# Kernel optimization log

Measured on AMD Instinct MI355X. Metric: run time of the kernel, lower is better.

The kernel has to match this reference:

```python
import jax, jax.numpy as jnp
import numpy as np

B, D, H1, H2, E, O = 32768, 256, 512, 256, 16, 64


def setup_inputs() -> dict:
    key = jax.random.key(0)
    ks = jax.random.split(key, 12)
    s = lambda fan_in: 1.0 / np.sqrt(fan_in)
    return {
        "x": jax.random.normal(ks[0], (B, D), dtype=jnp.float32),
        "gate_w": jax.random.normal(ks[1], (D, E), dtype=jnp.float32) * s(D),
        "gate_b": jnp.zeros((E,), dtype=jnp.float32),
        "W1": jax.random.normal(ks[2], (E, D, H1), dtype=jnp.float32) * s(D),
        "b1": jnp.zeros((E, H1), dtype=jnp.float32),
        "W2": jax.random.normal(ks[3], (E, H1, H2), dtype=jnp.float32) * s(H1),
        "b2": jnp.zeros((E, H2), dtype=jnp.float32),
        "W3": jax.random.normal(ks[4], (E, H2, O), dtype=jnp.float32) * s(H2),
        "b3": jnp.zeros((E, O), dtype=jnp.float32),
        "head_w": jax.random.normal(ks[5], (O, 1), dtype=jnp.float32) * s(O),
        "head_b": jnp.zeros((1,), dtype=jnp.float32),
    }


def reference(x, gate_w, gate_b, W1, b1, W2, b2, W3, b3, head_w, head_b):
    # gating: softmax over experts, [B, E]
    gates = jax.nn.softmax(x @ gate_w + gate_b, axis=-1)
    # all-expert dense MLP as batched GEMMs over leading expert axis
    h1 = jax.nn.relu(jnp.einsum('bd,edh->ebh', x, W1) + b1[:, None, :])   # [E,B,H1]
    h2 = jax.nn.relu(jnp.einsum('ebh,ehk->ebk', h1, W2) + b2[:, None, :])  # [E,B,H2]
    eo = jnp.einsum('ebk,eko->ebo', h2, W3) + b3[:, None, :]               # [E,B,O]
    # gated combination: sum_e gates[b,e] * eo[e,b,:]
    fused = jnp.einsum('be,ebo->bo', gates, eo)                            # [B,O]
    yts = (fused @ head_w + head_b)[:, 0]                                  # [B]
    return yts
```

## Files before the change

kernel.cpp:

```cpp
#include <hip/hip_runtime.h>

#define B_TOK 32768
#define D_IN  256
#define H1D   512
#define H2D   256
#define NE    16
#define NO    64

typedef _Float16 half8 __attribute__((ext_vector_type(8)));
typedef _Float16 half4 __attribute__((ext_vector_type(4)));
typedef float   float4_t __attribute__((ext_vector_type(4)));

__global__ void pack_w1(const float* __restrict__ W1, _Float16* __restrict__ w1p) {
  int t = blockIdx.x * 256 + threadIdx.x;
  int lane = t & 63;
  int kt   = (t >> 6) & 7;
  int ntg  = (t >> 9) & 31;
  int e    = t >> 14;
  int n  = ntg * 16 + (lane & 15);
  int kb = kt * 32 + (lane >> 4) * 8;
  half8 v;
  #pragma unroll
  for (int j = 0; j < 8; ++j)
    v[j] = (_Float16)W1[((size_t)(e * D_IN + kb + j)) * H1D + n];
  *(half8*)(w1p + (size_t)t * 8) = v;
}

__global__ void pack_w2(const float* __restrict__ W2, _Float16* __restrict__ w2p) {
  int t = blockIdx.x * 256 + threadIdx.x;
  int lane = t & 63;
  int ktg  = (t >> 6) & 15;
  int ntg  = (t >> 10) & 15;
  int e    = t >> 14;
  int n  = ntg * 16 + (lane & 15);
  int kb = ktg * 32 + (lane >> 4) * 8;
  half8 v;
  #pragma unroll
  for (int j = 0; j < 8; ++j)
    v[j] = (_Float16)W2[((size_t)(e * H1D + kb + j)) * H2D + n];
  *(half8*)(w2p + (size_t)t * 8) = v;
}

__global__ void pack_gate(const float* __restrict__ gw, _Float16* __restrict__ gwp) {
  int t = threadIdx.x;
  int lane = t & 63;
  int kt   = t >> 6;
  int e  = lane & 15;
  int kb = kt * 32 + (lane >> 4) * 8;
  half8 v;
  #pragma unroll
  for (int j = 0; j < 8; ++j)
    v[j] = (_Float16)gw[(kb + j) * NE + e];
  *(half8*)(gwp + (size_t)t * 8) = v;
}

__global__ void w3h_kernel(const float* __restrict__ W3, const float* __restrict__ b3,
                           const float* __restrict__ hw, float* __restrict__ w3h,
                           float* __restrict__ c3) {
  int t = blockIdx.x * 256 + threadIdx.x;
  if (t < NE * H2D) {
    int e = t >> 8, h = t & 255;
    float s = 0.f;
    #pragma unroll
    for (int o = 0; o < NO; ++o) s = fmaf(W3[((size_t)(e * H2D + h)) * NO + o], hw[o], s);
    w3h[t] = s;
  } else if (t < NE * H2D + NE) {
    int e = t - NE * H2D;
    float s = 0.f;
    #pragma unroll
    for (int o = 0; o < NO; ++o) s = fmaf(b3[e * NO + o], hw[o], s);
    c3[e] = s;
  }
}

#define H1STR 520

__global__ __launch_bounds__(256, 2) void moe_main(
    const float* __restrict__ x,
    const float* __restrict__ b1,
    const float* __restrict__ b2,
    const _Float16* __restrict__ w1p,
    const _Float16* __restrict__ w2p,
    const _Float16* __restrict__ gwp,
    const float* __restrict__ gb,
    const float* __restrict__ w3h,
    const float* __restrict__ c3,
    const float* __restrict__ head_b,
    float* __restrict__ out) {
  __shared__ _Float16 h1_lds[64 * H1STR];
  __shared__ float g_lds[NE * 68];
  __shared__ float fin[4 * 64];

  const int tid  = threadIdx.x;
  const int w    = tid >> 6;
  const int lane = tid & 63;
  const int q    = lane >> 4;
  const int l16  = lane & 15;
  const int m0   = blockIdx.x * 64;
  const int tok_lane = (l16 >> 2) * 16 + q * 4 + (l16 & 3);

  half8 xf[4][8];
  #pragma unroll
  for (int nt = 0; nt < 4; ++nt) {
    const float* xr = x + (size_t)(m0 + nt * 16 + l16) * D_IN + q * 8;
    #pragma unroll
    for (int kt = 0; kt < 8; ++kt) {
      float4_t v0 = *(const float4_t*)(xr + kt * 32);
      float4_t v1 = *(const float4_t*)(xr + kt * 32 + 4);
      half8 h;
      h[0] = (_Float16)v0[0]; h[1] = (_Float16)v0[1];
      h[2] = (_Float16)v0[2]; h[3] = (_Float16)v0[3];
      h[4] = (_Float16)v1[0]; h[5] = (_Float16)v1[1];
      h[6] = (_Float16)v1[2]; h[7] = (_Float16)v1[3];
      xf[nt][kt] = h;
    }
  }

  {
    float gbv = gb[l16];
    #pragma unroll
    for (int mt = 0; mt < 4; ++mt) {
      if (mt == w) {
        float4_t lg = (float4_t){0.f, 0.f, 0.f, 0.f};
        #pragma unroll
        for (int kt = 0; kt < 8; ++kt) {
          half8 bfr = *(const half8*)(gwp + (size_t)kt * 512 + lane * 8);
          lg = __builtin_amdgcn_mfma_f32_16x16x32_f16(xf[mt][kt], bfr, lg, 0, 0, 0);
        }
        #pragma unroll
        for (int r = 0; r < 4; ++r) {
          float v = lg[r] + gbv;
          float m = v;
          m = fmaxf(m, __shfl_xor(m, 1));
          m = fmaxf(m, __shfl_xor(m, 2));
          m = fmaxf(m, __shfl_xor(m, 4));
          m = fmaxf(m, __shfl_xor(m, 8));
          float p = __expf(v - m);
          float s = p;
          s += __shfl_xor(s, 1);
          s += __shfl_xor(s, 2);
          s += __shfl_xor(s, 4);
          s += __shfl_xor(s, 8);
          g_lds[l16 * 68 + mt * 16 + q * 4 + r] = p / s;
        }
      }
    }
  }

  float yacc = 0.f;

  for (int e = 0; e < NE; ++e) {
    #pragma unroll
    for (int ch = 0; ch < 2; ++ch) {
      float4_t a1[4][4];
      #pragma unroll
      for (int mt = 0; mt < 4; ++mt)
        #pragma unroll
        for (int nt = 0; nt < 4; ++nt)
          a1[mt][nt] = (float4_t){0.f, 0.f, 0.f, 0.f};

      const _Float16* wbase =
          w1p + ((size_t)((e * 32 + ch * 16 + w * 4) * 8)) * 512 + lane * 8;
      #pragma unroll
      for (int kt = 0; kt < 8; ++kt) {
        half8 wc[4];
        #pragma unroll
        for (int mt = 0; mt < 4; ++mt)
          wc[mt] = *(const half8*)(wbase + (size_t)(mt * 8 + kt) * 512);
        #pragma unroll
        for (int mt = 0; mt < 4; ++mt)
          #pragma unroll
          for (int nt = 0; nt < 4; ++nt)
            a1[mt][nt] = __builtin_amdgcn_mfma_f32_16x16x32_f16(
                wc[mt], xf[nt][kt], a1[mt][nt], 0, 0, 0);
      }

      #pragma unroll
      for (int mt = 0; mt < 4; ++mt) {
        int colbase = ch * 256 + (w * 4 + mt) * 16 + q * 4;
        float4_t bb = *(const float4_t*)(b1 + e * H1D + colbase);
        #pragma unroll
        for (int nt = 0; nt < 4; ++nt) {
          half4 hv;
          #pragma unroll
          for (int r = 0; r < 4; ++r)
            hv[r] = (_Float16)fmaxf(a1[mt][nt][r] + bb[r], 0.f);
          *(half4*)(h1_lds + (nt * 16 + l16) * H1STR + colbase) = hv;
        }
      }
    }
    __syncthreads();

    float4_t h2[4][4];
    #pragma unroll
    for (int mt = 0; mt < 4; ++mt)
      #pragma unroll
      for (int nt = 0; nt < 4; ++nt)
        h2[mt][nt] = (float4_t){0.f, 0.f, 0.f, 0.f};

    const _Float16* w2base =
        w2p + ((size_t)((e * 16 + w * 4) * 16)) * 512 + lane * 8;
    #pragma unroll
    for (int kt = 0; kt < 16; ++kt) {
      half8 w2c[4];
      #pragma unroll
      for (int nt = 0; nt < 4; ++nt)
        w2c[nt] = *(const half8*)(w2base + (size_t)(nt * 16 + kt) * 512);
      half8 hac[4];
      #pragma unroll
      for (int mt = 0; mt < 4; ++mt)
        hac[mt] = *(const half8*)(h1_lds + (mt * 16 + l16) * H1STR + kt * 32 + q * 8);
      #pragma unroll
      for (int mt = 0; mt < 4; ++mt)
        #pragma unroll
        for (int nt = 0; nt < 4; ++nt)
          h2[mt][nt] = __builtin_amdgcn_mfma_f32_16x16x32_f16(
              hac[mt], w2c[nt], h2[mt][nt], 0, 0, 0);
    }

    float b2v[4], w3v[4];
    #pragma unroll
    for (int nt = 0; nt < 4; ++nt) {
      int n = w * 64 + nt * 16 + l16;
      b2v[nt] = b2[e * H2D + n];
      w3v[nt] = w3h[e * H2D + n];
    }
    float s[4][4];
    #pragma unroll
    for (int mt = 0; mt < 4; ++mt)
      #pragma unroll
      for (int r = 0; r < 4; ++r) s[mt][r] = 0.f;
    #pragma unroll
    for (int mt = 0; mt < 4; ++mt)
      #pragma unroll
      for (int nt = 0; nt < 4; ++nt)
        #pragma unroll
        for (int r = 0; r < 4; ++r)
          s[mt][r] += fmaxf(h2[mt][nt][r] + b2v[nt], 0.f) * w3v[nt];

    float ge = g_lds[e * 68 + tok_lane];
    #pragma unroll
    for (int i = 0; i < 16; ++i) {
      float v = s[i >> 2][i & 3];
      v += __shfl_xor(v, 1);
      v += __shfl_xor(v, 2);
      v += __shfl_xor(v, 4);
      v += __shfl_xor(v, 8);
      if (l16 == i) yacc += ge * v;
    }
    __syncthreads();
  }

  fin[w * 64 + tok_lane] = yacc;
  __syncthreads();
  if (tid < 64) {
    float sum = fin[tid] + fin[64 + tid] + fin[128 + tid] + fin[192 + tid];
    float gc = 0.f;
    #pragma unroll
    for (int e = 0; e < NE; ++e) gc += g_lds[e * 68 + tid] * c3[e];
    out[m0 + tid] = sum + gc + head_b[0];
  }
}

extern "C" void kernel_launch(void* const* d_in, const int* in_sizes, int n_in,
                              void* d_out, int out_size, void* d_ws, size_t ws_size,
                              hipStream_t stream) {
  const float* x      = (const float*)d_in[0];
  const float* gate_w = (const float*)d_in[1];
  const float* gate_b = (const float*)d_in[2];
  const float* W1     = (const float*)d_in[3];
  const float* b1     = (const float*)d_in[4];
  const float* W2     = (const float*)d_in[5];
  const float* b2     = (const float*)d_in[6];
  const float* W3     = (const float*)d_in[7];
  const float* b3     = (const float*)d_in[8];
  const float* head_w = (const float*)d_in[9];
  const float* head_b = (const float*)d_in[10];
  float* out = (float*)d_out;

  char* ws = (char*)d_ws;
  _Float16* w1p = (_Float16*)(ws);
  _Float16* w2p = (_Float16*)(ws + 4194304);
  _Float16* gwp = (_Float16*)(ws + 8388608);
  float*    w3h = (float*)(ws + 8396800);
  float*    c3  = (float*)(ws + 8413184);

  hipLaunchKernelGGL(pack_w1, dim3(1024), dim3(256), 0, stream, W1, w1p);
  hipLaunchKernelGGL(pack_w2, dim3(1024), dim3(256), 0, stream, W2, w2p);
  hipLaunchKernelGGL(pack_gate, dim3(1), dim3(512), 0, stream, gate_w, gwp);
  hipLaunchKernelGGL(w3h_kernel, dim3(17), dim3(256), 0, stream,
                     W3, b3, head_w, w3h, c3);
  hipLaunchKernelGGL(moe_main, dim3(B_TOK / 64), dim3(256), 0, stream,
                     x, b1, b2, w1p, w2p, gwp, gate_b, w3h, c3, head_b, out);
}
```

Baseline: 412.4 us.

## Use eight waves per block with double-buffered H1 and register prefetch

```diff
diff --git a/kernel.cpp b/kernel.cpp
--- a/kernel.cpp
+++ b/kernel.cpp
@@ -75,7 +75,7 @@
 
 #define H1STR 520
 
-__global__ __launch_bounds__(256, 2) void moe_main(
+__global__ __launch_bounds__(512, 2) void moe_main(
     const float* __restrict__ x,
     const float* __restrict__ b1,
     const float* __restrict__ b2,
@@ -87,9 +87,9 @@
     const float* __restrict__ c3,
     const float* __restrict__ head_b,
     float* __restrict__ out) {
-  __shared__ _Float16 h1_lds[64 * H1STR];
+  __shared__ _Float16 h1_lds[2][64 * H1STR];
   __shared__ float g_lds[NE * 68];
-  __shared__ float fin[4 * 64];
+  __shared__ float fin[8 * 64];
 
   const int tid  = threadIdx.x;
   const int w    = tid >> 6;
@@ -116,7 +116,7 @@
     }
   }
 
-  {
+  if (w < 4) {
     float gbv = gb[l16];
     #pragma unroll
     for (int mt = 0; mt < 4; ++mt) {
@@ -149,79 +149,99 @@
 
   float yacc = 0.f;
 
+  const _Float16* w1base = w1p + ((size_t)(w * 4 * 8)) * 512 + lane * 8;
+  const _Float16* w2base = w2p + ((size_t)(w * 2 * 16)) * 512 + lane * 8;
+
   for (int e = 0; e < NE; ++e) {
-    #pragma unroll
-    for (int ch = 0; ch < 2; ++ch) {
-      float4_t a1[4][4];
+    _Float16* h1b = h1_lds[e & 1];
+    const _Float16* w1e = w1base + (size_t)e * (32 * 8 * 512);
+    const _Float16* w2e = w2base + (size_t)e * (16 * 16 * 512);
+
+    float4_t a1[4][4];
+    #pragma unroll
+    for (int mt = 0; mt < 4; ++mt)
+      #pragma unroll
+      for (int nt = 0; nt < 4; ++nt)
+        a1[mt][nt] = (float4_t){0.f, 0.f, 0.f, 0.f};
+
+    half8 wc[4], wn[4];
+    #pragma unroll
+    for (int mt = 0; mt < 4; ++mt)
+      wc[mt] = *(const half8*)(w1e + (size_t)(mt * 8 + 0) * 512);
+    #pragma unroll
+    for (int kt = 0; kt < 8; ++kt) {
+      if (kt < 7) {
+        #pragma unroll
+        for (int mt = 0; mt < 4; ++mt)
+          wn[mt] = *(const half8*)(w1e + (size_t)(mt * 8 + kt + 1) * 512);
+      }
       #pragma unroll
       for (int mt = 0; mt < 4; ++mt)
         #pragma unroll
         for (int nt = 0; nt < 4; ++nt)
-          a1[mt][nt] = (float4_t){0.f, 0.f, 0.f, 0.f};
-
-      const _Float16* wbase =
-          w1p + ((size_t)((e * 32 + ch * 16 + w * 4) * 8)) * 512 + lane * 8;
-      #pragma unroll
-      for (int kt = 0; kt < 8; ++kt) {
-        half8 wc[4];
+          a1[mt][nt] = __builtin_amdgcn_mfma_f32_16x16x32_f16(
+              wc[mt], xf[nt][kt], a1[mt][nt], 0, 0, 0);
+      #pragma unroll
+      for (int mt = 0; mt < 4; ++mt) wc[mt] = wn[mt];
+    }
+
+    #pragma unroll
+    for (int mt = 0; mt < 4; ++mt) {
+      int colbase = (w * 4 + mt) * 16 + q * 4;
+      float4_t bb = *(const float4_t*)(b1 + e * H1D + colbase);
+      #pragma unroll
+      for (int nt = 0; nt < 4; ++nt) {
+        half4 hv;
+        #pragma unroll
+        for (int r = 0; r < 4; ++r)
+          hv[r] = (_Float16)fmaxf(a1[mt][nt][r] + bb[r], 0.f);
+        *(half4*)(h1b + (nt * 16 + l16) * H1STR + colbase) = hv;
+      }
+    }
+
+    __syncthreads();
+
+    float4_t h2[4][2];
+    #pragma unroll
+    for (int mt = 0; mt < 4; ++mt)
+      #pragma unroll
+      for (int nt = 0; nt < 2; ++nt)
+        h2[mt][nt] = (float4_t){0.f, 0.f, 0.f, 0.f};
+
+    half8 w2c[2], w2n[2], hac[4], han[4];
+    #pragma unroll
+    for (int nt = 0; nt < 2; ++nt)
+      w2c[nt] = *(const half8*)(w2e + (size_t)(nt * 16 + 0) * 512);
+    #pragma unroll
+    for (int mt = 0; mt < 4; ++mt)
+      hac[mt] = *(const half8*)(h1b + (mt * 16 + l16) * H1STR + 0 * 32 + q * 8);
+
+    #pragma unroll
+    for (int kt = 0; kt < 16; ++kt) {
+      if (kt < 15) {
+        #pragma unroll
+        for (int nt = 0; nt < 2; ++nt)
+          w2n[nt] = *(const half8*)(w2e + (size_t)(nt * 16 + kt + 1) * 512);
         #pragma unroll
         for (int mt = 0; mt < 4; ++mt)
-          wc[mt] = *(const half8*)(wbase + (size_t)(mt * 8 + kt) * 512);
-        #pragma unroll
-        for (int mt = 0; mt < 4; ++mt)
-          #pragma unroll
-          for (int nt = 0; nt < 4; ++nt)
-            a1[mt][nt] = __builtin_amdgcn_mfma_f32_16x16x32_f16(
-                wc[mt], xf[nt][kt], a1[mt][nt], 0, 0, 0);
+          han[mt] = *(const half8*)(h1b + (mt * 16 + l16) * H1STR + (kt + 1) * 32 + q * 8);
       }
-
-      #pragma unroll
-      for (int mt = 0; mt < 4; ++mt) {
-        int colbase = ch * 256 + (w * 4 + mt) * 16 + q * 4;
-        float4_t bb = *(const float4_t*)(b1 + e * H1D + colbase);
-        #pragma unroll
-        for (int nt = 0; nt < 4; ++nt) {
-          half4 hv;
-          #pragma unroll
-          for (int r = 0; r < 4; ++r)
-            hv[r] = (_Float16)fmaxf(a1[mt][nt][r] + bb[r], 0.f);
-          *(half4*)(h1_lds + (nt * 16 + l16) * H1STR + colbase) = hv;
-        }
-      }
-    }
-    __syncthreads();
-
-    float4_t h2[4][4];
-    #pragma unroll
-    for (int mt = 0; mt < 4; ++mt)
-      #pragma unroll
-      for (int nt = 0; nt < 4; ++nt)
-        h2[mt][nt] = (float4_t){0.f, 0.f, 0.f, 0.f};
-
-    const _Float16* w2base =
-        w2p + ((size_t)((e * 16 + w * 4) * 16)) * 512 + lane * 8;
-    #pragma unroll
-    for (int kt = 0; kt < 16; ++kt) {
-      half8 w2c[4];
-      #pragma unroll
-      for (int nt = 0; nt < 4; ++nt)
-        w2c[nt] = *(const half8*)(w2base + (size_t)(nt * 16 + kt) * 512);
-      half8 hac[4];
       #pragma unroll
       for (int mt = 0; mt < 4; ++mt)
-        hac[mt] = *(const half8*)(h1_lds + (mt * 16 + l16) * H1STR + kt * 32 + q * 8);
-      #pragma unroll
-      for (int mt = 0; mt < 4; ++mt)
-        #pragma unroll
-        for (int nt = 0; nt < 4; ++nt)
+        #pragma unroll
+        for (int nt = 0; nt < 2; ++nt)
           h2[mt][nt] = __builtin_amdgcn_mfma_f32_16x16x32_f16(
               hac[mt], w2c[nt], h2[mt][nt], 0, 0, 0);
-    }
-
-    float b2v[4], w3v[4];
-    #pragma unroll
-    for (int nt = 0; nt < 4; ++nt) {
-      int n = w * 64 + nt * 16 + l16;
+      #pragma unroll
+      for (int nt = 0; nt < 2; ++nt) w2c[nt] = w2n[nt];
+      #pragma unroll
+      for (int mt = 0; mt < 4; ++mt) hac[mt] = han[mt];
+    }
+
+    float b2v[2], w3v[2];
+    #pragma unroll
+    for (int nt = 0; nt < 2; ++nt) {
+      int n = w * 32 + nt * 16 + l16;
       b2v[nt] = b2[e * H2D + n];
       w3v[nt] = w3h[e * H2D + n];
     }
@@ -233,7 +253,7 @@
     #pragma unroll
     for (int mt = 0; mt < 4; ++mt)
       #pragma unroll
-      for (int nt = 0; nt < 4; ++nt)
+      for (int nt = 0; nt < 2; ++nt)
         #pragma unroll
         for (int r = 0; r < 4; ++r)
           s[mt][r] += fmaxf(h2[mt][nt][r] + b2v[nt], 0.f) * w3v[nt];
@@ -248,13 +268,14 @@
       v += __shfl_xor(v, 8);
       if (l16 == i) yacc += ge * v;
     }
-    __syncthreads();
   }
 
   fin[w * 64 + tok_lane] = yacc;
   __syncthreads();
   if (tid < 64) {
-    float sum = fin[tid] + fin[64 + tid] + fin[128 + tid] + fin[192 + tid];
+    float sum = 0.f;
+    #pragma unroll
+    for (int k = 0; k < 8; ++k) sum += fin[k * 64 + tid];
     float gc = 0.f;
     #pragma unroll
     for (int e = 0; e < NE; ++e) gc += g_lds[e * 68 + tid] * c3[e];
@@ -290,6 +311,6 @@
   hipLaunchKernelGGL(pack_gate, dim3(1), dim3(512), 0, stream, gate_w, gwp);
   hipLaunchKernelGGL(w3h_kernel, dim3(17), dim3(256), 0, stream,
                      W3, b3, head_w, w3h, c3);
-  hipLaunchKernelGGL(moe_main, dim3(B_TOK / 64), dim3(256), 0, stream,
+  hipLaunchKernelGGL(moe_main, dim3(B_TOK / 64), dim3(512), 0, stream,
                      x, b1, b2, w1p, w2p, gwp, gate_b, w3h, c3, head_b, out);
 }
```

Result: slower. 485.4 us (+17.7%).

## Use 128-token tiles with 16-wave blocks and merge prep kernels

Applied to the files above, without the earlier changes.

```diff
diff --git a/kernel.cpp b/kernel.cpp
--- a/kernel.cpp
+++ b/kernel.cpp
@@ -6,76 +6,79 @@
 #define H2D   256
 #define NE    16
 #define NO    64
+#define TK    128
 
 typedef _Float16 half8 __attribute__((ext_vector_type(8)));
 typedef _Float16 half4 __attribute__((ext_vector_type(4)));
 typedef float   float4_t __attribute__((ext_vector_type(4)));
 
-__global__ void pack_w1(const float* __restrict__ W1, _Float16* __restrict__ w1p) {
-  int t = blockIdx.x * 256 + threadIdx.x;
-  int lane = t & 63;
-  int kt   = (t >> 6) & 7;
-  int ntg  = (t >> 9) & 31;
-  int e    = t >> 14;
-  int n  = ntg * 16 + (lane & 15);
-  int kb = kt * 32 + (lane >> 4) * 8;
-  half8 v;
-  #pragma unroll
-  for (int j = 0; j < 8; ++j)
-    v[j] = (_Float16)W1[((size_t)(e * D_IN + kb + j)) * H1D + n];
-  *(half8*)(w1p + (size_t)t * 8) = v;
+__global__ void prep_kernel(const float* __restrict__ W1, const float* __restrict__ W2,
+                            const float* __restrict__ W3, const float* __restrict__ b3,
+                            const float* __restrict__ hw, const float* __restrict__ gw,
+                            _Float16* __restrict__ w1p, _Float16* __restrict__ w2p,
+                            float* __restrict__ w3h, float* __restrict__ c3,
+                            _Float16* __restrict__ gwp) {
+  int blk = blockIdx.x;
+  int tid = threadIdx.x;
+  if (blk < 1024) {
+    int t = blk * 256 + tid;
+    int lane = t & 63;
+    int kt   = (t >> 6) & 7;
+    int ntg  = (t >> 9) & 31;
+    int e    = t >> 14;
+    int n  = ntg * 16 + (lane & 15);
+    int kb = kt * 32 + (lane >> 4) * 8;
+    half8 v;
+    #pragma unroll
+    for (int j = 0; j < 8; ++j)
+      v[j] = (_Float16)W1[((size_t)(e * D_IN + kb + j)) * H1D + n];
+    *(half8*)(w1p + (size_t)t * 8) = v;
+  } else if (blk < 2048) {
+    int t = (blk - 1024) * 256 + tid;
+    int lane = t & 63;
+    int ktg  = (t >> 6) & 15;
+    int ntg  = (t >> 10) & 15;
+    int e    = t >> 14;
+    int n  = ntg * 16 + (lane & 15);
+    int kb = ktg * 32 + (lane >> 4) * 8;
+    half8 v;
+    #pragma unroll
+    for (int j = 0; j < 8; ++j)
+      v[j] = (_Float16)W2[((size_t)(e * H1D + kb + j)) * H2D + n];
+    *(half8*)(w2p + (size_t)t * 8) = v;
+  } else if (blk < 2065) {
+    int t = (blk - 2048) * 256 + tid;
+    if (t < NE * H2D) {
+      int e = t >> 8, h = t & 255;
+      float s = 0.f;
+      #pragma unroll
+      for (int o = 0; o < NO; ++o) s = fmaf(W3[((size_t)(e * H2D + h)) * NO + o], hw[o], s);
+      w3h[t] = s;
+    } else if (t < NE * H2D + NE) {
+      int e = t - NE * H2D;
+      float s = 0.f;
+      #pragma unroll
+      for (int o = 0; o < NO; ++o) s = fmaf(b3[e * NO + o], hw[o], s);
+      c3[e] = s;
+    }
+  } else {
+    for (int t = tid; t < 512; t += 256) {
+      int lane = t & 63;
+      int kt   = t >> 6;
+      int e  = lane & 15;
+      int kb = kt * 32 + (lane >> 4) * 8;
+      half8 v;
+      #pragma unroll
+      for (int j = 0; j < 8; ++j)
+        v[j] = (_Float16)gw[(kb + j) * NE + e];
+      *(half8*)(gwp + (size_t)t * 8) = v;
+    }
+  }
 }
 
-__global__ void pack_w2(const float* __restrict__ W2, _Float16* __restrict__ w2p) {
-  int t = blockIdx.x * 256 + threadIdx.x;
-  int lane = t & 63;
-  int ktg  = (t >> 6) & 15;
-  int ntg  = (t >> 10) & 15;
-  int e    = t >> 14;
-  int n  = ntg * 16 + (lane & 15);
-  int kb = ktg * 32 + (lane >> 4) * 8;
-  half8 v;
-  #pragma unroll
-  for (int j = 0; j < 8; ++j)
-    v[j] = (_Float16)W2[((size_t)(e * H1D + kb + j)) * H2D + n];
-  *(half8*)(w2p + (size_t)t * 8) = v;
-}
-
-__global__ void pack_gate(const float* __restrict__ gw, _Float16* __restrict__ gwp) {
-  int t = threadIdx.x;
-  int lane = t & 63;
-  int kt   = t >> 6;
-  int e  = lane & 15;
-  int kb = kt * 32 + (lane >> 4) * 8;
-  half8 v;
-  #pragma unroll
-  for (int j = 0; j < 8; ++j)
-    v[j] = (_Float16)gw[(kb + j) * NE + e];
-  *(half8*)(gwp + (size_t)t * 8) = v;
-}
-
-__global__ void w3h_kernel(const float* __restrict__ W3, const float* __restrict__ b3,
-                           const float* __restrict__ hw, float* __restrict__ w3h,
-                           float* __restrict__ c3) {
-  int t = blockIdx.x * 256 + threadIdx.x;
-  if (t < NE * H2D) {
-    int e = t >> 8, h = t & 255;
-    float s = 0.f;
-    #pragma unroll
-    for (int o = 0; o < NO; ++o) s = fmaf(W3[((size_t)(e * H2D + h)) * NO + o], hw[o], s);
-    w3h[t] = s;
-  } else if (t < NE * H2D + NE) {
-    int e = t - NE * H2D;
-    float s = 0.f;
-    #pragma unroll
-    for (int o = 0; o < NO; ++o) s = fmaf(b3[e * NO + o], hw[o], s);
-    c3[e] = s;
-  }
-}
-
 #define H1STR 520
 
-__global__ __launch_bounds__(256, 2) void moe_main(
+__global__ __launch_bounds__(1024, 4) void moe_main(
     const float* __restrict__ x,
     const float* __restrict__ b1,
     const float* __restrict__ b2,
@@ -87,22 +90,23 @@
     const float* __restrict__ c3,
     const float* __restrict__ head_b,
     float* __restrict__ out) {
-  __shared__ _Float16 h1_lds[64 * H1STR];
-  __shared__ float g_lds[NE * 68];
-  __shared__ float fin[4 * 64];
+  __shared__ _Float16 h1_lds[TK * H1STR];
+  __shared__ float g_lds[TK * 17];
+  __shared__ float fin[4 * TK];
 
   const int tid  = threadIdx.x;
   const int w    = tid >> 6;
   const int lane = tid & 63;
   const int q    = lane >> 4;
   const int l16  = lane & 15;
-  const int m0   = blockIdx.x * 64;
-  const int tok_lane = (l16 >> 2) * 16 + q * 4 + (l16 & 3);
-
-  half8 xf[4][8];
+  const int tp   = w >> 2;
+  const int ng   = w & 3;
+  const int m0   = blockIdx.x * TK;
+
+  half8 xf[2][8];
   #pragma unroll
-  for (int nt = 0; nt < 4; ++nt) {
-    const float* xr = x + (size_t)(m0 + nt * 16 + l16) * D_IN + q * 8;
+  for (int mi = 0; mi < 2; ++mi) {
+    const float* xr = x + (size_t)(m0 + (2 * tp + mi) * 16 + l16) * D_IN + q * 8;
     #pragma unroll
     for (int kt = 0; kt < 8; ++kt) {
       float4_t v0 = *(const float4_t*)(xr + kt * 32);
@@ -112,152 +116,157 @@
       h[2] = (_Float16)v0[2]; h[3] = (_Float16)v0[3];
       h[4] = (_Float16)v1[0]; h[5] = (_Float16)v1[1];
       h[6] = (_Float16)v1[2]; h[7] = (_Float16)v1[3];
-      xf[nt][kt] = h;
-    }
-  }
-
-  {
+      xf[mi][kt] = h;
+    }
+  }
+
+  if (ng == 0) {
     float gbv = gb[l16];
     #pragma unroll
-    for (int mt = 0; mt < 4; ++mt) {
-      if (mt == w) {
-        float4_t lg = (float4_t){0.f, 0.f, 0.f, 0.f};
-        #pragma unroll
-        for (int kt = 0; kt < 8; ++kt) {
-          half8 bfr = *(const half8*)(gwp + (size_t)kt * 512 + lane * 8);
-          lg = __builtin_amdgcn_mfma_f32_16x16x32_f16(xf[mt][kt], bfr, lg, 0, 0, 0);
-        }
-        #pragma unroll
-        for (int r = 0; r < 4; ++r) {
-          float v = lg[r] + gbv;
-          float m = v;
-          m = fmaxf(m, __shfl_xor(m, 1));
-          m = fmaxf(m, __shfl_xor(m, 2));
-          m = fmaxf(m, __shfl_xor(m, 4));
-          m = fmaxf(m, __shfl_xor(m, 8));
-          float p = __expf(v - m);
-          float s = p;
-          s += __shfl_xor(s, 1);
-          s += __shfl_xor(s, 2);
-          s += __shfl_xor(s, 4);
-          s += __shfl_xor(s, 8);
-          g_lds[l16 * 68 + mt * 16 + q * 4 + r] = p / s;
-        }
-      }
-    }
-  }
-
-  float yacc = 0.f;
+    for (int mi = 0; mi < 2; ++mi) {
+      float4_t lg = (float4_t){0.f, 0.f, 0.f, 0.f};
+      #pragma unroll
+      for (int kt = 0; kt < 8; ++kt) {
+        half8 bfr = *(const half8*)(gwp + (size_t)kt * 512 + lane * 8);
+        lg = __builtin_amdgcn_mfma_f32_16x16x32_f16(xf[mi][kt], bfr, lg, 0, 0, 0);
+      }
+      #pragma unroll
+      for (int r = 0; r < 4; ++r) {
+        float v = lg[r] + gbv;
+        float m = v;
+        m = fmaxf(m, __shfl_xor(m, 1));
+        m = fmaxf(m, __shfl_xor(m, 2));
+        m = fmaxf(m, __shfl_xor(m, 4));
+        m = fmaxf(m, __shfl_xor(m, 8));
+        float p = __expf(v - m);
+        float s = p;
+        s += __shfl_xor(s, 1);
+        s += __shfl_xor(s, 2);
+        s += __shfl_xor(s, 4);
+        s += __shfl_xor(s, 8);
+        int tok = (2 * tp + mi) * 16 + q * 4 + r;
+        g_lds[tok * 17 + l16] = p / s;
+      }
+    }
+  }
+
+  float yacc[2][4];
+  #pragma unroll
+  for (int mi = 0; mi < 2; ++mi)
+    #pragma unroll
+    for (int r = 0; r < 4; ++r) yacc[mi][r] = 0.f;
 
   for (int e = 0; e < NE; ++e) {
     #pragma unroll
-    for (int ch = 0; ch < 2; ++ch) {
-      float4_t a1[4][4];
-      #pragma unroll
-      for (int mt = 0; mt < 4; ++mt)
+    for (int nh = 0; nh < 2; ++nh) {
+      float4_t a1[2][4];
+      #pragma unroll
+      for (int mi = 0; mi < 2; ++mi)
         #pragma unroll
         for (int nt = 0; nt < 4; ++nt)
-          a1[mt][nt] = (float4_t){0.f, 0.f, 0.f, 0.f};
-
-      const _Float16* wbase =
-          w1p + ((size_t)((e * 32 + ch * 16 + w * 4) * 8)) * 512 + lane * 8;
+          a1[mi][nt] = (float4_t){0.f, 0.f, 0.f, 0.f};
+
+      const _Float16* w1e =
+          w1p + ((size_t)((e * 32 + ng * 8 + nh * 4) * 8)) * 512 + lane * 8;
       #pragma unroll
       for (int kt = 0; kt < 8; ++kt) {
         half8 wc[4];
         #pragma unroll
-        for (int mt = 0; mt < 4; ++mt)
-          wc[mt] = *(const half8*)(wbase + (size_t)(mt * 8 + kt) * 512);
-        #pragma unroll
-        for (int mt = 0; mt < 4; ++mt)
+        for (int nt = 0; nt < 4; ++nt)
+          wc[nt] = *(const half8*)(w1e + (size_t)(nt * 8 + kt) * 512);
+        #pragma unroll
+        for (int mi = 0; mi < 2; ++mi)
           #pragma unroll
           for (int nt = 0; nt < 4; ++nt)
-            a1[mt][nt] = __builtin_amdgcn_mfma_f32_16x16x32_f16(
-                wc[mt], xf[nt][kt], a1[mt][nt], 0, 0, 0);
-      }
-
-      #pragma unroll
-      for (int mt = 0; mt < 4; ++mt) {
-        int colbase = ch * 256 + (w * 4 + mt) * 16 + q * 4;
+            a1[mi][nt] = __builtin_amdgcn_mfma_f32_16x16x32_f16(
+                wc[nt], xf[mi][kt], a1[mi][nt], 0, 0, 0);
+      }
+
+      #pragma unroll
+      for (int nt = 0; nt < 4; ++nt) {
+        int colbase = (ng * 8 + nh * 4 + nt) * 16 + q * 4;
         float4_t bb = *(const float4_t*)(b1 + e * H1D + colbase);
         #pragma unroll
-        for (int nt = 0; nt < 4; ++nt) {
+        for (int mi = 0; mi < 2; ++mi) {
           half4 hv;
           #pragma unroll
           for (int r = 0; r < 4; ++r)
-            hv[r] = (_Float16)fmaxf(a1[mt][nt][r] + bb[r], 0.f);
-          *(half4*)(h1_lds + (nt * 16 + l16) * H1STR + colbase) = hv;
+            hv[r] = (_Float16)fmaxf(a1[mi][nt][r] + bb[r], 0.f);
+          *(half4*)(h1_lds + ((2 * tp + mi) * 16 + l16) * H1STR + colbase) = hv;
         }
       }
     }
+
     __syncthreads();
 
-    float4_t h2[4][4];
-    #pragma unroll
-    for (int mt = 0; mt < 4; ++mt)
+    float4_t h2[2][4];
+    #pragma unroll
+    for (int mi = 0; mi < 2; ++mi)
       #pragma unroll
       for (int nt = 0; nt < 4; ++nt)
-        h2[mt][nt] = (float4_t){0.f, 0.f, 0.f, 0.f};
-
-    const _Float16* w2base =
-        w2p + ((size_t)((e * 16 + w * 4) * 16)) * 512 + lane * 8;
+        h2[mi][nt] = (float4_t){0.f, 0.f, 0.f, 0.f};
+
+    const _Float16* w2e =
+        w2p + ((size_t)((e * 16 + ng * 4) * 16)) * 512 + lane * 8;
     #pragma unroll
     for (int kt = 0; kt < 16; ++kt) {
+      half8 hac[2];
+      #pragma unroll
+      for (int mi = 0; mi < 2; ++mi)
+        hac[mi] = *(const half8*)(h1_lds + ((2 * tp + mi) * 16 + l16) * H1STR + kt * 32 + q * 8);
       half8 w2c[4];
       #pragma unroll
       for (int nt = 0; nt < 4; ++nt)
-        w2c[nt] = *(const half8*)(w2base + (size_t)(nt * 16 + kt) * 512);
-      half8 hac[4];
-      #pragma unroll
-      for (int mt = 0; mt < 4; ++mt)
-        hac[mt] = *(const half8*)(h1_lds + (mt * 16 + l16) * H1STR + kt * 32 + q * 8);
-      #pragma unroll
-      for (int mt = 0; mt < 4; ++mt)
+        w2c[nt] = *(const half8*)(w2e + (size_t)(nt * 16 + kt) * 512);
+      #pragma unroll
+      for (int mi = 0; mi < 2; ++mi)
         #pragma unroll
         for (int nt = 0; nt < 4; ++nt)
-          h2[mt][nt] = __builtin_amdgcn_mfma_f32_16x16x32_f16(
-              hac[mt], w2c[nt], h2[mt][nt], 0, 0, 0);
+          h2[mi][nt] = __builtin_amdgcn_mfma_f32_16x16x32_f16(
+              hac[mi], w2c[nt], h2[mi][nt], 0, 0, 0);
     }
 
     float b2v[4], w3v[4];
     #pragma unroll
     for (int nt = 0; nt < 4; ++nt) {
-      int n = w * 64 + nt * 16 + l16;
+      int n = (ng * 4 + nt) * 16 + l16;
       b2v[nt] = b2[e * H2D + n];
       w3v[nt] = w3h[e * H2D + n];
     }
-    float s[4][4];
-    #pragma unroll
-    for (int mt = 0; mt < 4; ++mt)
-      #pragma unroll
-      for (int r = 0; r < 4; ++r) s[mt][r] = 0.f;
-    #pragma unroll
-    for (int mt = 0; mt < 4; ++mt)
-      #pragma unroll
-      for (int nt = 0; nt < 4; ++nt)
-        #pragma unroll
-        for (int r = 0; r < 4; ++r)
-          s[mt][r] += fmaxf(h2[mt][nt][r] + b2v[nt], 0.f) * w3v[nt];
-
-    float ge = g_lds[e * 68 + tok_lane];
-    #pragma unroll
-    for (int i = 0; i < 16; ++i) {
-      float v = s[i >> 2][i & 3];
+    #pragma unroll
+    for (int mi = 0; mi < 2; ++mi) {
+      #pragma unroll
+      for (int r = 0; r < 4; ++r) {
+        float s = 0.f;
+        #pragma unroll
+        for (int nt = 0; nt < 4; ++nt)
+          s += fmaxf(h2[mi][nt][r] + b2v[nt], 0.f) * w3v[nt];
+        int tok = (2 * tp + mi) * 16 + q * 4 + r;
+        yacc[mi][r] += g_lds[tok * 17 + e] * s;
+      }
+    }
+    __syncthreads();
+  }
+
+  #pragma unroll
+  for (int mi = 0; mi < 2; ++mi) {
+    #pragma unroll
+    for (int r = 0; r < 4; ++r) {
+      float v = yacc[mi][r];
       v += __shfl_xor(v, 1);
       v += __shfl_xor(v, 2);
       v += __shfl_xor(v, 4);
       v += __shfl_xor(v, 8);
-      if (l16 == i) yacc += ge * v;
-    }
-    __syncthreads();
-  }
-
-  fin[w * 64 + tok_lane] = yacc;
+      if (l16 == 0)
+        fin[ng * TK + (2 * tp + mi) * 16 + q * 4 + r] = v;
+    }
+  }
   __syncthreads();
-  if (tid < 64) {
-    float sum = fin[tid] + fin[64 + tid] + fin[128 + tid] + fin[192 + tid];
+  if (tid < TK) {
+    float sum = fin[tid] + fin[TK + tid] + fin[2 * TK + tid] + fin[3 * TK + tid];
     float gc = 0.f;
     #pragma unroll
-    for (int e = 0; e < NE; ++e) gc += g_lds[e * 68 + tid] * c3[e];
+    for (int e = 0; e < NE; ++e) gc += g_lds[tid * 17 + e] * c3[e];
     out[m0 + tid] = sum + gc + head_b[0];
   }
 }
@@ -285,11 +294,8 @@
   float*    w3h = (float*)(ws + 8396800);
   float*    c3  = (float*)(ws + 8413184);
 
-  hipLaunchKernelGGL(pack_w1, dim3(1024), dim3(256), 0, stream, W1, w1p);
-  hipLaunchKernelGGL(pack_w2, dim3(1024), dim3(256), 0, stream, W2, w2p);
-  hipLaunchKernelGGL(pack_gate, dim3(1), dim3(512), 0, stream, gate_w, gwp);
-  hipLaunchKernelGGL(w3h_kernel, dim3(17), dim3(256), 0, stream,
-                     W3, b3, head_w, w3h, c3);
-  hipLaunchKernelGGL(moe_main, dim3(B_TOK / 64), dim3(256), 0, stream,
+  hipLaunchKernelGGL(prep_kernel, dim3(2066), dim3(256), 0, stream,
+                     W1, W2, W3, b3, head_w, gate_w, w1p, w2p, w3h, c3, gwp);
+  hipLaunchKernelGGL(moe_main, dim3(B_TOK / TK), dim3(1024), 0, stream,
                      x, b1, b2, w1p, w2p, gwp, gate_b, w3h, c3, head_b, out);
 }
```

Measured after the change: 660.4 us. 60.1% more time.
